# Optimization experiments

Measured on AMD Instinct MI355X. Metric: run time of the kernel, lower is better.

The kernel has to match this reference:

```python
import jax, jax.numpy as jnp
import numpy as np

NUM_HEADS = 16
NUM_HIDDENS = 1024
NEG_INF = -1e6


def setup_inputs() -> dict:
    key = jax.random.key(0)
    ks = jax.random.split(key, 8)
    B, S, D = 2, 2048, NUM_HIDDENS
    scale = 1.0 / np.sqrt(D)
    return {
        "q": jax.random.normal(ks[0], (B, S, D), jnp.float32),
        "k": jax.random.normal(ks[1], (B, S, D), jnp.float32),
        "v": jax.random.normal(ks[2], (B, S, D), jnp.float32),
        # nn.Linear weights have shape (out_features, in_features)
        "Wq": jax.random.normal(ks[3], (D, D), jnp.float32) * scale,
        "Wk": jax.random.normal(ks[4], (D, D), jnp.float32) * scale,
        "Wv": jax.random.normal(ks[5], (D, D), jnp.float32) * scale,
        "Wo": jax.random.normal(ks[6], (D, D), jnp.float32) * scale,
        "valid_len": jax.random.randint(ks[7], (B,), 1, 2048 + 1, jnp.int32),
    }


def _unpack_heads(x, nh):
    # (B, S, H) -> (B*nh, S, H//nh), matching Unpack_base_head
    B, S, H = x.shape
    return x.reshape(B, S, nh, H // nh).transpose(0, 2, 1, 3).reshape(B * nh, S, H // nh)


def _merge_heads(x, nh):
    # Faithful to Merge_base_head: (B*nh, S, dh) -> (B, nh, S, dh)
    # -> permute(0,2,3,1) -> (B, S, dh, nh) -> (B, S, dh*nh)
    Bnh, S, dh = x.shape
    B = Bnh // nh
    x = x.reshape(B, nh, S, dh).transpose(0, 2, 3, 1)
    return x.reshape(B, S, dh * nh)


def reference(q, k, v, Wq, Wk, Wv, Wo, valid_len):
    nh = NUM_HEADS
    # projections (bias=False); Linear: x @ W.T
    qh = _unpack_heads(q @ Wq.T, nh)  # (B*nh, S, dh)
    kh = _unpack_heads(k @ Wk.T, nh)
    vh = _unpack_heads(v @ Wv.T, nh)
    dh = qh.shape[-1]
    scores = jnp.einsum("bqd,bkd->bqk", qh, kh) / jnp.sqrt(jnp.float32(dh))
    # repeat_interleave valid_len by num_heads along dim 0
    vl = jnp.repeat(valid_len, nh)  # (B*nh,)
    key_pos = jnp.arange(scores.shape[-1])  # (S,)
    mask = key_pos[None, None, :] < vl[:, None, None]  # (B*nh, 1, S)
    scores = jnp.where(mask, scores, NEG_INF)
    attn = jax.nn.softmax(scores, axis=-1)  # dropout=0.0 (eval) -> identity
    out = jnp.einsum("bqk,bkd->bqd", attn, vh)  # (B*nh, S, dh)
    out = _merge_heads(out, nh) @ Wo.T  # (B, S, H)
    return out, attn
```

## Files before the change

### kernel.cpp

```cpp
#include <hip/hip_runtime.h>
#include <stdint.h>

#define SB 2048
#define DB 1024
#define NHB 16
#define DHB 64

typedef __attribute__((ext_vector_type(8))) short short8;
typedef __attribute__((ext_vector_type(4))) float f32x4;

__device__ __forceinline__ unsigned short f2bf(float f) {
  union { float f; uint32_t u; } v; v.f = f;
  uint32_t u = v.u;
  return (unsigned short)((u + 0x7FFFu + ((u >> 16) & 1u)) >> 16);
}

__device__ __forceinline__ void gld16(const void* g, void* l) {
  __builtin_amdgcn_global_load_lds(
      (const __attribute__((address_space(1))) void*)g,
      (__attribute__((address_space(3))) void*)l, 16, 0, 0);
}

__device__ __forceinline__ int xcd_swz(int bid, int nwg) {
  return (bid & 7) * (nwg >> 3) + (bid >> 3);
}

struct ConvArgs {
  const float* s[7];
  unsigned short* d[7];
  int n[7];
};

__global__ __launch_bounds__(256) void conv_kernel(ConvArgs a) {
  const int t = blockIdx.y;
  const float* __restrict__ src = a.s[t];
  unsigned short* __restrict__ dst = a.d[t];
  const int n8 = a.n[t] >> 3;
  for (int i = blockIdx.x * 256 + threadIdx.x; i < n8; i += gridDim.x * 256) {
    const f32x4* p = (const f32x4*)src + (size_t)i * 2;
    f32x4 x = p[0], y = p[1];
    short8 o;
    o[0] = (short)f2bf(x[0]); o[1] = (short)f2bf(x[1]);
    o[2] = (short)f2bf(x[2]); o[3] = (short)f2bf(x[3]);
    o[4] = (short)f2bf(y[0]); o[5] = (short)f2bf(y[1]);
    o[6] = (short)f2bf(y[2]); o[7] = (short)f2bf(y[3]);
    *(short8*)(dst + (size_t)i * 8) = o;
  }
}

struct ProjArgs {
  const unsigned short* A[3];
  const unsigned short* B[3];
  unsigned short* O[3];
};

__global__ __launch_bounds__(256) void proj_gemm(ProjArgs pa) {
  __shared__ unsigned short SH[12288];
  unsigned short* Ab = SH;
  unsigned short* Bb = SH + 8192;

  const int z = blockIdx.y;
  const unsigned short* __restrict__ A = pa.A[z];
  const unsigned short* __restrict__ Bw = pa.B[z];
  unsigned short* __restrict__ O = pa.O[z];

  const int tid = threadIdx.x;
  const int w = tid >> 6, lane = tid & 63;
  const int g = lane >> 4, li = lane & 15;
  const int wm = w >> 1, wn = w & 1;
  const int l = xcd_swz(blockIdx.x, 512);
  const int m0 = (l >> 4) * 128, n0 = (l & 15) * 64;

  const int srow = lane >> 3;
  const int sg = (lane & 7) ^ srow;

  int a_off[4][2], b_off[2][2];
  #pragma unroll
  for (int mf = 0; mf < 4; ++mf) {
    int row = wm * 64 + mf * 16 + li;
    #pragma unroll
    for (int ks = 0; ks < 2; ++ks)
      a_off[mf][ks] = row * 64 + (((ks * 4 + g) ^ (li & 7)) << 3);
  }
  #pragma unroll
  for (int nf = 0; nf < 2; ++nf) {
    int row = wn * 32 + nf * 16 + li;
    #pragma unroll
    for (int ks = 0; ks < 2; ++ks)
      b_off[nf][ks] = row * 64 + (((ks * 4 + g) ^ (li & 7)) << 3);
  }

  f32x4 acc[4][2];
  #pragma unroll
  for (int i = 0; i < 4; ++i)
    #pragma unroll
    for (int j = 0; j < 2; ++j)
      #pragma unroll
      for (int e = 0; e < 4; ++e) acc[i][j][e] = 0.f;

  for (int k0 = 0; k0 < DB; k0 += 64) {
    __syncthreads();
    #pragma unroll
    for (int i = 0; i < 4; ++i) {
      int c = w * 4 + i;
      gld16(A + (size_t)(m0 + c * 8 + srow) * DB + k0 + sg * 8, Ab + c * 512);
    }
    #pragma unroll
    for (int i = 0; i < 2; ++i) {
      int c = w * 2 + i;
      gld16(Bw + (size_t)(n0 + c * 8 + srow) * DB + k0 + sg * 8, Bb + c * 512);
    }
    __syncthreads();
    short8 af[4][2], bf[2][2];
    #pragma unroll
    for (int mf = 0; mf < 4; ++mf)
      #pragma unroll
      for (int ks = 0; ks < 2; ++ks)
        af[mf][ks] = *(const short8*)&Ab[a_off[mf][ks]];
    #pragma unroll
    for (int nf = 0; nf < 2; ++nf)
      #pragma unroll
      for (int ks = 0; ks < 2; ++ks)
        bf[nf][ks] = *(const short8*)&Bb[b_off[nf][ks]];
    #pragma unroll
    for (int ks = 0; ks < 2; ++ks)
      #pragma unroll
      for (int mf = 0; mf < 4; ++mf)
        #pragma unroll
        for (int nf = 0; nf < 2; ++nf)
          acc[mf][nf] = __builtin_amdgcn_mfma_f32_16x16x32_bf16(
              af[mf][ks], bf[nf][ks], acc[mf][nf], 0, 0, 0);
  }

  const int h = n0 >> 6;
  if (z < 2) {
    #pragma unroll
    for (int mf = 0; mf < 4; ++mf)
      #pragma unroll
      for (int nf = 0; nf < 2; ++nf)
        #pragma unroll
        for (int r = 0; r < 4; ++r) {
          int row = m0 + wm * 64 + mf * 16 + g * 4 + r;
          int col = n0 + wn * 32 + nf * 16 + li;
          int b_ = row >> 11, s_ = row & 2047, dp = col & 63;
          O[((size_t)(b_ * NHB + h) * SB + s_) * DHB + dp] = f2bf(acc[mf][nf][r]);
        }
  } else {
    __syncthreads();
    #pragma unroll
    for (int mf = 0; mf < 4; ++mf)
      #pragma unroll
      for (int nf = 0; nf < 2; ++nf)
        #pragma unroll
        for (int r = 0; r < 4; ++r)
          SH[(wm * 64 + mf * 16 + g * 4 + r) * 72 + wn * 32 + nf * 16 + li] =
              f2bf(acc[mf][nf][r]);
    __syncthreads();
    int dp = tid >> 2, ss = tid & 3;
    int b_ = m0 >> 11, s0 = (m0 & 2047) + ss * 32;
    unsigned short* dst = O + ((size_t)(b_ * NHB + h) * DHB + dp) * SB + s0;
    #pragma unroll
    for (int j2 = 0; j2 < 4; ++j2) {
      short8 o;
      #pragma unroll
      for (int j = 0; j < 8; ++j) o[j] = (short)SH[(ss * 32 + j2 * 8 + j) * 72 + dp];
      *(short8*)(dst + j2 * 8) = o;
    }
  }
}

__global__ __launch_bounds__(256) void attn_kernel(
    const unsigned short* __restrict__ Qh, const unsigned short* __restrict__ Kh,
    const unsigned short* __restrict__ Vt, const int* __restrict__ valid_len,
    float* __restrict__ attn_out, unsigned short* __restrict__ Mg)
{
  __shared__ unsigned short Klds[64][72];
  __shared__ unsigned short Vlds[64][72];
  __shared__ unsigned short QP[128][72];

  const int tid = threadIdx.x;
  const int wave = tid >> 6, lane = tid & 63;
  const int g = lane >> 4, li = lane & 15;
  const int lsw = xcd_swz(blockIdx.x, 512);
  const int q0 = (lsw & 15) * 128;
  const int bh = lsw >> 4;
  const int b_ = bh >> 4;
  const int vl = valid_len[b_];
  const int nkt = min(32, (vl + 63) >> 6);

  {
    int qr = tid >> 1, half = (tid & 1) * 32;
    const unsigned short* src = Qh + ((size_t)bh * SB + q0 + qr) * DHB + half;
    #pragma unroll
    for (int j = 0; j < 4; ++j)
      *(short8*)&QP[qr][half + j * 8] = *(const short8*)(src + j * 8);
  }
  __syncthreads();

  short8 qa[2][2];
  #pragma unroll
  for (int qf = 0; qf < 2; ++qf)
    #pragma unroll
    for (int ks = 0; ks < 2; ++ks)
      qa[qf][ks] = *(const short8*)&QP[wave * 32 + qf * 16 + li][ks * 32 + g * 8];

  float mrow[2][4], lrow[2][4];
  #pragma unroll
  for (int qf = 0; qf < 2; ++qf)
    #pragma unroll
    for (int r = 0; r < 4; ++r) { mrow[qf][r] = -1e30f; lrow[qf][r] = 0.f; }

  for (int kti = 0; kti < nkt; ++kti) {
    const int kt = kti * 64;
    __syncthreads();
    {
      int kr = tid >> 2, cs = (tid & 3) * 16;
      const unsigned short* src = Kh + ((size_t)bh * SB + kt + kr) * DHB + cs;
      *(short8*)&Klds[kr][cs]     = *(const short8*)src;
      *(short8*)&Klds[kr][cs + 8] = *(const short8*)(src + 8);
    }
    __syncthreads();
    f32x4 sc[2][4];
    #pragma unroll
    for (int qf = 0; qf < 2; ++qf)
      #pragma unroll
      for (int nf = 0; nf < 4; ++nf)
        #pragma unroll
        for (int j = 0; j < 4; ++j) sc[qf][nf][j] = 0.f;
    #pragma unroll
    for (int ks = 0; ks < 2; ++ks)
      #pragma unroll
      for (int nf = 0; nf < 4; ++nf) {
        short8 kb = *(const short8*)&Klds[nf * 16 + li][ks * 32 + g * 8];
        #pragma unroll
        for (int qf = 0; qf < 2; ++qf)
          sc[qf][nf] = __builtin_amdgcn_mfma_f32_16x16x32_bf16(qa[qf][ks], kb, sc[qf][nf], 0, 0, 0);
      }
    #pragma unroll
    for (int qf = 0; qf < 2; ++qf)
      #pragma unroll
      for (int r = 0; r < 4; ++r) {
        float sv[4], tm = -1e30f;
        #pragma unroll
        for (int nf = 0; nf < 4; ++nf) {
          int key = kt + nf * 16 + li;
          float s = sc[qf][nf][r] * 0.125f;
          s = (key < vl) ? s : -1e6f;
          sv[nf] = s;
          tm = fmaxf(tm, s);
        }
        float mo = mrow[qf][r];
        float mn = fmaxf(mo, tm);
        float la = lrow[qf][r] * __expf(mo - mn);
        #pragma unroll
        for (int nf = 0; nf < 4; ++nf) la += __expf(sv[nf] - mn);
        lrow[qf][r] = la;
        mrow[qf][r] = mn;
      }
  }

  float rl[2][4];
  #pragma unroll
  for (int qf = 0; qf < 2; ++qf)
    #pragma unroll
    for (int r = 0; r < 4; ++r) {
      float M = mrow[qf][r];
      #pragma unroll
      for (int d = 1; d < 16; d <<= 1) M = fmaxf(M, __shfl_xor(M, d));
      float L = lrow[qf][r] * __expf(mrow[qf][r] - M);
      #pragma unroll
      for (int d = 1; d < 16; d <<= 1) L += __shfl_xor(L, d);
      mrow[qf][r] = M;
      rl[qf][r] = 1.f / L;
    }

  f32x4 oacc[2][4];
  #pragma unroll
  for (int qf = 0; qf < 2; ++qf)
    #pragma unroll
    for (int nf = 0; nf < 4; ++nf)
      #pragma unroll
      for (int j = 0; j < 4; ++j) oacc[qf][nf][j] = 0.f;

  for (int kti = 0; kti < nkt; ++kti) {
    const int kt = kti * 64;
    __syncthreads();
    {
      int kr = tid >> 2, cs = (tid & 3) * 16;
      const unsigned short* src = Kh + ((size_t)bh * SB + kt + kr) * DHB + cs;
      *(short8*)&Klds[kr][cs]     = *(const short8*)src;
      *(short8*)&Klds[kr][cs + 8] = *(const short8*)(src + 8);
      const unsigned short* vs = Vt + ((size_t)bh * DHB + kr) * SB + kt + cs;
      *(short8*)&Vlds[kr][cs]     = *(const short8*)vs;
      *(short8*)&Vlds[kr][cs + 8] = *(const short8*)(vs + 8);
    }
    __syncthreads();
    f32x4 sc[2][4];
    #pragma unroll
    for (int qf = 0; qf < 2; ++qf)
      #pragma unroll
      for (int nf = 0; nf < 4; ++nf)
        #pragma unroll
        for (int j = 0; j < 4; ++j) sc[qf][nf][j] = 0.f;
    #pragma unroll
    for (int ks = 0; ks < 2; ++ks)
      #pragma unroll
      for (int nf = 0; nf < 4; ++nf) {
        short8 kb = *(const short8*)&Klds[nf * 16 + li][ks * 32 + g * 8];
        #pragma unroll
        for (int qf = 0; qf < 2; ++qf)
          sc[qf][nf] = __builtin_amdgcn_mfma_f32_16x16x32_bf16(qa[qf][ks], kb, sc[qf][nf], 0, 0, 0);
      }
    #pragma unroll
    for (int qf = 0; qf < 2; ++qf)
      #pragma unroll
      for (int nf = 0; nf < 4; ++nf)
        #pragma unroll
        for (int r = 0; r < 4; ++r) {
          int key = kt + nf * 16 + li;
          float s = sc[qf][nf][r] * 0.125f;
          s = (key < vl) ? s : -1e6f;
          float p = __expf(s - mrow[qf][r]) * rl[qf][r];
          int qrow = q0 + wave * 32 + qf * 16 + g * 4 + r;
          __builtin_nontemporal_store(
              p, attn_out + (size_t)bh * SB * SB + (size_t)qrow * SB + key);
          QP[wave * 32 + qf * 16 + g * 4 + r][nf * 16 + li] = f2bf(p);
        }
    __syncthreads();
    #pragma unroll
    for (int ks = 0; ks < 2; ++ks) {
      short8 vb[4];
      #pragma unroll
      for (int nf = 0; nf < 4; ++nf)
        vb[nf] = *(const short8*)&Vlds[nf * 16 + li][ks * 32 + g * 8];
      #pragma unroll
      for (int qf = 0; qf < 2; ++qf) {
        short8 pa = *(const short8*)&QP[wave * 32 + qf * 16 + li][ks * 32 + g * 8];
        #pragma unroll
        for (int nf = 0; nf < 4; ++nf)
          oacc[qf][nf] = __builtin_amdgcn_mfma_f32_16x16x32_bf16(pa, vb[nf], oacc[qf][nf], 0, 0, 0);
      }
    }
  }

  {
    int c0 = nkt * 64;
    int rem4 = (SB - c0) >> 2;
    if (rem4 > 0) {
      f32x4 z;
      z[0] = 0.f; z[1] = 0.f; z[2] = 0.f; z[3] = 0.f;
      for (int row = 0; row < 128; ++row) {
        float* dst = attn_out + (size_t)bh * SB * SB + (size_t)(q0 + row) * SB + c0;
        for (int c = tid; c < rem4; c += 256)
          __builtin_nontemporal_store(z, (f32x4*)dst + c);
      }
    }
  }

  const int h = bh & 15;
  #pragma unroll
  for (int qf = 0; qf < 2; ++qf)
    #pragma unroll
    for (int nf = 0; nf < 4; ++nf)
      #pragma unroll
      for (int r = 0; r < 4; ++r) {
        int qrow = q0 + wave * 32 + qf * 16 + g * 4 + r;
        int dp = nf * 16 + li;
        Mg[((size_t)b_ * SB + qrow) * DB + dp * NHB + h] = f2bf(oacc[qf][nf][r]);
      }
}

__global__ __launch_bounds__(256) void out_gemm(
    const unsigned short* __restrict__ A, const unsigned short* __restrict__ Bw,
    float* __restrict__ Out)
{
  __shared__ unsigned short SH[12288];
  unsigned short* Ab = SH;
  unsigned short* Bb = SH + 8192;

  const int tid = threadIdx.x;
  const int w = tid >> 6, lane = tid & 63;
  const int g = lane >> 4, li = lane & 15;
  const int wm = w >> 1, wn = w & 1;
  const int l = xcd_swz(blockIdx.x, 512);
  const int m0 = (l >> 4) * 128, n0 = (l & 15) * 64;

  const int srow = lane >> 3;
  const int sg = (lane & 7) ^ srow;

  int a_off[4][2], b_off[2][2];
  #pragma unroll
  for (int mf = 0; mf < 4; ++mf) {
    int row = wm * 64 + mf * 16 + li;
    #pragma unroll
    for (int ks = 0; ks < 2; ++ks)
      a_off[mf][ks] = row * 64 + (((ks * 4 + g) ^ (li & 7)) << 3);
  }
  #pragma unroll
  for (int nf = 0; nf < 2; ++nf) {
    int row = wn * 32 + nf * 16 + li;
    #pragma unroll
    for (int ks = 0; ks < 2; ++ks)
      b_off[nf][ks] = row * 64 + (((ks * 4 + g) ^ (li & 7)) << 3);
  }

  f32x4 acc[4][2];
  #pragma unroll
  for (int i = 0; i < 4; ++i)
    #pragma unroll
    for (int j = 0; j < 2; ++j)
      #pragma unroll
      for (int e = 0; e < 4; ++e) acc[i][j][e] = 0.f;

  for (int k0 = 0; k0 < DB; k0 += 64) {
    __syncthreads();
    #pragma unroll
    for (int i = 0; i < 4; ++i) {
      int c = w * 4 + i;
      gld16(A + (size_t)(m0 + c * 8 + srow) * DB + k0 + sg * 8, Ab + c * 512);
    }
    #pragma unroll
    for (int i = 0; i < 2; ++i) {
      int c = w * 2 + i;
      gld16(Bw + (size_t)(n0 + c * 8 + srow) * DB + k0 + sg * 8, Bb + c * 512);
    }
    __syncthreads();
    short8 af[4][2], bf[2][2];
    #pragma unroll
    for (int mf = 0; mf < 4; ++mf)
      #pragma unroll
      for (int ks = 0; ks < 2; ++ks)
        af[mf][ks] = *(const short8*)&Ab[a_off[mf][ks]];
    #pragma unroll
    for (int nf = 0; nf < 2; ++nf)
      #pragma unroll
      for (int ks = 0; ks < 2; ++ks)
        bf[nf][ks] = *(const short8*)&Bb[b_off[nf][ks]];
    #pragma unroll
    for (int ks = 0; ks < 2; ++ks)
      #pragma unroll
      for (int mf = 0; mf < 4; ++mf)
        #pragma unroll
        for (int nf = 0; nf < 2; ++nf)
          acc[mf][nf] = __builtin_amdgcn_mfma_f32_16x16x32_bf16(
              af[mf][ks], bf[nf][ks], acc[mf][nf], 0, 0, 0);
  }

  #pragma unroll
  for (int mf = 0; mf < 4; ++mf)
    #pragma unroll
    for (int nf = 0; nf < 2; ++nf)
      #pragma unroll
      for (int r = 0; r < 4; ++r) {
        int row = m0 + wm * 64 + mf * 16 + g * 4 + r;
        int col = n0 + wn * 32 + nf * 16 + li;
        Out[(size_t)row * DB + col] = acc[mf][nf][r];
      }
}

extern "C" void kernel_launch(void* const* d_in, const int* in_sizes, int n_in,
                              void* d_out, int out_size, void* d_ws, size_t ws_size,
                              hipStream_t stream) {
  const float* q  = (const float*)d_in[0];
  const float* k  = (const float*)d_in[1];
  const float* v  = (const float*)d_in[2];
  const float* Wq = (const float*)d_in[3];
  const float* Wk = (const float*)d_in[4];
  const float* Wv = (const float*)d_in[5];
  const float* Wo = (const float*)d_in[6];
  const int* vlen = (const int*)d_in[7];

  const size_t HS = (size_t)2 * NHB * SB * DHB;
  const size_t WS = (size_t)DB * DB;

  unsigned short* ws = (unsigned short*)d_ws;
  unsigned short* qb  = ws;
  unsigned short* kb  = qb + HS;
  unsigned short* vb  = kb + HS;
  unsigned short* Wqb = vb + HS;
  unsigned short* Wkb = Wqb + WS;
  unsigned short* Wvb = Wkb + WS;
  unsigned short* Wob = Wvb + WS;
  unsigned short* Qh  = Wob + WS;
  unsigned short* Kh  = Qh + HS;
  unsigned short* Vt  = Kh + HS;
  unsigned short* Mg  = qb;

  float* out  = (float*)d_out;
  float* attn = out + (size_t)2 * SB * DB;

  ConvArgs ca;
  ca.s[0] = q;  ca.d[0] = qb;  ca.n[0] = (int)HS;
  ca.s[1] = k;  ca.d[1] = kb;  ca.n[1] = (int)HS;
  ca.s[2] = v;  ca.d[2] = vb;  ca.n[2] = (int)HS;
  ca.s[3] = Wq; ca.d[3] = Wqb; ca.n[3] = (int)WS;
  ca.s[4] = Wk; ca.d[4] = Wkb; ca.n[4] = (int)WS;
  ca.s[5] = Wv; ca.d[5] = Wvb; ca.n[5] = (int)WS;
  ca.s[6] = Wo; ca.d[6] = Wob; ca.n[6] = (int)WS;

  ProjArgs pa;
  pa.A[0] = qb;  pa.A[1] = kb;  pa.A[2] = vb;
  pa.B[0] = Wqb; pa.B[1] = Wkb; pa.B[2] = Wvb;
  pa.O[0] = Qh;  pa.O[1] = Kh;  pa.O[2] = Vt;

  dim3 blk(256);
  conv_kernel<<<dim3(1024, 7), blk, 0, stream>>>(ca);
  proj_gemm<<<dim3(512, 3), blk, 0, stream>>>(pa);
  attn_kernel<<<dim3(512), blk, 0, stream>>>(Qh, Kh, Vt, vlen, attn, Mg);
  out_gemm<<<dim3(512), blk, 0, stream>>>(Mg, Wob, out);
}
```

Baseline: 248.9 us.

## Unify GEMMs into 128x128 tiles and pipeline attention K/V loads

```diff
diff --git a/kernel.cpp b/kernel.cpp
--- a/kernel.cpp
+++ b/kernel.cpp
@@ -7,6 +7,7 @@
 #define DHB 64
 
 typedef __attribute__((ext_vector_type(8))) short short8;
+typedef __attribute__((ext_vector_type(4))) short short4v;
 typedef __attribute__((ext_vector_type(4))) float f32x4;
 
 __device__ __forceinline__ unsigned short f2bf(float f) {
@@ -48,53 +49,38 @@
   }
 }
 
-struct ProjArgs {
+struct GemmArgs {
   const unsigned short* A[3];
   const unsigned short* B[3];
-  unsigned short* O[3];
+  void* O[3];
+  int mode[3];
 };
 
-__global__ __launch_bounds__(256) void proj_gemm(ProjArgs pa) {
-  __shared__ unsigned short SH[12288];
+__global__ __launch_bounds__(256) void gemm128(GemmArgs ga) {
+  __shared__ unsigned short SH[17408];
   unsigned short* Ab = SH;
   unsigned short* Bb = SH + 8192;
 
   const int z = blockIdx.y;
-  const unsigned short* __restrict__ A = pa.A[z];
-  const unsigned short* __restrict__ Bw = pa.B[z];
-  unsigned short* __restrict__ O = pa.O[z];
+  const unsigned short* __restrict__ A = ga.A[z];
+  const unsigned short* __restrict__ Bw = ga.B[z];
+  const int mode = ga.mode[z];
 
   const int tid = threadIdx.x;
   const int w = tid >> 6, lane = tid & 63;
   const int g = lane >> 4, li = lane & 15;
   const int wm = w >> 1, wn = w & 1;
-  const int l = xcd_swz(blockIdx.x, 512);
-  const int m0 = (l >> 4) * 128, n0 = (l & 15) * 64;
+  const int l = xcd_swz(blockIdx.x, 256);
+  const int m0 = (l >> 3) * 128, n0 = (l & 7) * 128;
 
   const int srow = lane >> 3;
   const int sg = (lane & 7) ^ srow;
 
-  int a_off[4][2], b_off[2][2];
-  #pragma unroll
-  for (int mf = 0; mf < 4; ++mf) {
-    int row = wm * 64 + mf * 16 + li;
-    #pragma unroll
-    for (int ks = 0; ks < 2; ++ks)
-      a_off[mf][ks] = row * 64 + (((ks * 4 + g) ^ (li & 7)) << 3);
-  }
-  #pragma unroll
-  for (int nf = 0; nf < 2; ++nf) {
-    int row = wn * 32 + nf * 16 + li;
-    #pragma unroll
-    for (int ks = 0; ks < 2; ++ks)
-      b_off[nf][ks] = row * 64 + (((ks * 4 + g) ^ (li & 7)) << 3);
-  }
-
-  f32x4 acc[4][2];
+  f32x4 acc[4][4];
   #pragma unroll
   for (int i = 0; i < 4; ++i)
     #pragma unroll
-    for (int j = 0; j < 2; ++j)
+    for (int j = 0; j < 4; ++j)
       #pragma unroll
       for (int e = 0; e < 4; ++e) acc[i][j][e] = 0.f;
 
@@ -104,68 +90,80 @@
     for (int i = 0; i < 4; ++i) {
       int c = w * 4 + i;
       gld16(A + (size_t)(m0 + c * 8 + srow) * DB + k0 + sg * 8, Ab + c * 512);
-    }
-    #pragma unroll
-    for (int i = 0; i < 2; ++i) {
-      int c = w * 2 + i;
       gld16(Bw + (size_t)(n0 + c * 8 + srow) * DB + k0 + sg * 8, Bb + c * 512);
     }
     __syncthreads();
-    short8 af[4][2], bf[2][2];
+    short8 af[4][2], bf[4][2];
     #pragma unroll
     for (int mf = 0; mf < 4; ++mf)
       #pragma unroll
       for (int ks = 0; ks < 2; ++ks)
-        af[mf][ks] = *(const short8*)&Ab[a_off[mf][ks]];
-    #pragma unroll
-    for (int nf = 0; nf < 2; ++nf)
+        af[mf][ks] = *(const short8*)&Ab[(wm * 64 + mf * 16 + li) * 64 +
+                                         (((ks * 4 + g) ^ (li & 7)) << 3)];
+    #pragma unroll
+    for (int nf = 0; nf < 4; ++nf)
       #pragma unroll
       for (int ks = 0; ks < 2; ++ks)
-        bf[nf][ks] = *(const short8*)&Bb[b_off[nf][ks]];
+        bf[nf][ks] = *(const short8*)&Bb[(wn * 64 + nf * 16 + li) * 64 +
+                                         (((ks * 4 + g) ^ (li & 7)) << 3)];
     #pragma unroll
     for (int ks = 0; ks < 2; ++ks)
       #pragma unroll
       for (int mf = 0; mf < 4; ++mf)
         #pragma unroll
-        for (int nf = 0; nf < 2; ++nf)
+        for (int nf = 0; nf < 4; ++nf)
           acc[mf][nf] = __builtin_amdgcn_mfma_f32_16x16x32_bf16(
               af[mf][ks], bf[nf][ks], acc[mf][nf], 0, 0, 0);
   }
 
-  const int h = n0 >> 6;
-  if (z < 2) {
+  if (mode == 0) {
+    unsigned short* O = (unsigned short*)ga.O[z];
     #pragma unroll
     for (int mf = 0; mf < 4; ++mf)
       #pragma unroll
-      for (int nf = 0; nf < 2; ++nf)
+      for (int nf = 0; nf < 4; ++nf)
         #pragma unroll
         for (int r = 0; r < 4; ++r) {
           int row = m0 + wm * 64 + mf * 16 + g * 4 + r;
-          int col = n0 + wn * 32 + nf * 16 + li;
-          int b_ = row >> 11, s_ = row & 2047, dp = col & 63;
+          int col = n0 + wn * 64 + nf * 16 + li;
+          int b_ = row >> 11, s_ = row & 2047;
+          int h = col >> 6, dp = col & 63;
           O[((size_t)(b_ * NHB + h) * SB + s_) * DHB + dp] = f2bf(acc[mf][nf][r]);
         }
+  } else if (mode == 1) {
+    unsigned short* O = (unsigned short*)ga.O[z];
+    __syncthreads();
+    #pragma unroll
+    for (int mf = 0; mf < 4; ++mf)
+      #pragma unroll
+      for (int nf = 0; nf < 4; ++nf) {
+        short4v pk;
+        #pragma unroll
+        for (int r = 0; r < 4; ++r) pk[r] = (short)f2bf(acc[mf][nf][r]);
+        *(short4v*)&SH[(size_t)(wn * 64 + nf * 16 + li) * 136 +
+                       wm * 64 + mf * 16 + g * 4] = pk;
+      }
+    __syncthreads();
+    int c = tid >> 1, rh = tid & 1;
+    int col = n0 + c;
+    int h = col >> 6, dp = col & 63;
+    int b_ = m0 >> 11, s0 = (m0 & 2047) + rh * 64;
+    unsigned short* dst = O + ((size_t)(b_ * NHB + h) * DHB + dp) * SB + s0;
+    #pragma unroll
+    for (int j = 0; j < 8; ++j)
+      *(short8*)(dst + j * 8) = *(const short8*)&SH[c * 136 + rh * 64 + j * 8];
   } else {
-    __syncthreads();
+    float* O = (float*)ga.O[z];
     #pragma unroll
     for (int mf = 0; mf < 4; ++mf)
       #pragma unroll
-      for (int nf = 0; nf < 2; ++nf)
-        #pragma unroll
-        for (int r = 0; r < 4; ++r)
-          SH[(wm * 64 + mf * 16 + g * 4 + r) * 72 + wn * 32 + nf * 16 + li] =
-              f2bf(acc[mf][nf][r]);
-    __syncthreads();
-    int dp = tid >> 2, ss = tid & 3;
-    int b_ = m0 >> 11, s0 = (m0 & 2047) + ss * 32;
-    unsigned short* dst = O + ((size_t)(b_ * NHB + h) * DHB + dp) * SB + s0;
-    #pragma unroll
-    for (int j2 = 0; j2 < 4; ++j2) {
-      short8 o;
-      #pragma unroll
-      for (int j = 0; j < 8; ++j) o[j] = (short)SH[(ss * 32 + j2 * 8 + j) * 72 + dp];
-      *(short8*)(dst + j2 * 8) = o;
-    }
+      for (int nf = 0; nf < 4; ++nf)
+        #pragma unroll
+        for (int r = 0; r < 4; ++r) {
+          int row = m0 + wm * 64 + mf * 16 + g * 4 + r;
+          int col = n0 + wn * 64 + nf * 16 + li;
+          O[(size_t)row * DB + col] = acc[mf][nf][r];
+        }
   }
 }
 
@@ -174,8 +172,8 @@
     const unsigned short* __restrict__ Vt, const int* __restrict__ valid_len,
     float* __restrict__ attn_out, unsigned short* __restrict__ Mg)
 {
-  __shared__ unsigned short Klds[64][72];
-  __shared__ unsigned short Vlds[64][72];
+  __shared__ unsigned short Kb[2][4096];
+  __shared__ unsigned short Vb[2][4096];
   __shared__ unsigned short QP[128][72];
 
   const int tid = threadIdx.x;
@@ -188,6 +186,9 @@
   const int vl = valid_len[b_];
   const int nkt = min(32, (vl + 63) >> 6);
 
+  const int srow = lane >> 3;
+  const int sg = (lane & 7) ^ srow;
+
   {
     int qr = tid >> 1, half = (tid & 1) * 32;
     const unsigned short* src = Qh + ((size_t)bh * SB + q0 + qr) * DHB + half;
@@ -204,75 +205,84 @@
     for (int ks = 0; ks < 2; ++ks)
       qa[qf][ks] = *(const short8*)&QP[wave * 32 + qf * 16 + li][ks * 32 + g * 8];
 
-  float mrow[2][4], lrow[2][4];
+  float mQ[2] = {-1e30f, -1e30f}, lQ[2] = {0.f, 0.f};
+
+  {
+    #pragma unroll
+    for (int i = 0; i < 2; ++i) {
+      int c = wave * 2 + i;
+      gld16(Kh + ((size_t)bh * SB + 0 + c * 8 + srow) * DHB + sg * 8,
+            &Kb[0][c * 512]);
+    }
+    int cur = 0;
+    for (int kti = 0; kti < nkt; ++kti) {
+      const int kt = kti * 64;
+      __syncthreads();
+      if (kti + 1 < nkt) {
+        #pragma unroll
+        for (int i = 0; i < 2; ++i) {
+          int c = wave * 2 + i;
+          gld16(Kh + ((size_t)bh * SB + kt + 64 + c * 8 + srow) * DHB + sg * 8,
+                &Kb[cur ^ 1][c * 512]);
+        }
+      }
+      f32x4 sc[2][4];
+      #pragma unroll
+      for (int qf = 0; qf < 2; ++qf)
+        #pragma unroll
+        for (int nf = 0; nf < 4; ++nf)
+          #pragma unroll
+          for (int j = 0; j < 4; ++j) sc[qf][nf][j] = 0.f;
+      #pragma unroll
+      for (int ks = 0; ks < 2; ++ks)
+        #pragma unroll
+        for (int nf = 0; nf < 4; ++nf) {
+          short8 kbf = *(const short8*)&Kb[cur][(nf * 16 + li) * 64 +
+                                               (((ks * 4 + g) ^ (li & 7)) << 3)];
+          #pragma unroll
+          for (int qf = 0; qf < 2; ++qf)
+            sc[qf][nf] = __builtin_amdgcn_mfma_f32_16x16x32_bf16(
+                kbf, qa[qf][ks], sc[qf][nf], 0, 0, 0);
+        }
+      #pragma unroll
+      for (int qf = 0; qf < 2; ++qf) {
+        float tm = -1e30f;
+        #pragma unroll
+        for (int nf = 0; nf < 4; ++nf)
+          #pragma unroll
+          for (int r = 0; r < 4; ++r) {
+            int key = kt + nf * 16 + g * 4 + r;
+            float s = sc[qf][nf][r] * 0.125f;
+            s = (key < vl) ? s : -1e6f;
+            sc[qf][nf][r] = s;
+            tm = fmaxf(tm, s);
+          }
+        float mo = mQ[qf], mn = fmaxf(mo, tm);
+        float la = lQ[qf] * __expf(mo - mn);
+        #pragma unroll
+        for (int nf = 0; nf < 4; ++nf)
+          #pragma unroll
+          for (int r = 0; r < 4; ++r) la += __expf(sc[qf][nf][r] - mn);
+        mQ[qf] = mn;
+        lQ[qf] = la;
+      }
+      cur ^= 1;
+    }
+  }
+  __syncthreads();
+
+  float rlQ[2];
   #pragma unroll
-  for (int qf = 0; qf < 2; ++qf)
-    #pragma unroll
-    for (int r = 0; r < 4; ++r) { mrow[qf][r] = -1e30f; lrow[qf][r] = 0.f; }
-
-  for (int kti = 0; kti < nkt; ++kti) {
-    const int kt = kti * 64;
-    __syncthreads();
-    {
-      int kr = tid >> 2, cs = (tid & 3) * 16;
-      const unsigned short* src = Kh + ((size_t)bh * SB + kt + kr) * DHB + cs;
-      *(short8*)&Klds[kr][cs]     = *(const short8*)src;
-      *(short8*)&Klds[kr][cs + 8] = *(const short8*)(src + 8);
-    }
-    __syncthreads();
-    f32x4 sc[2][4];
-    #pragma unroll
-    for (int qf = 0; qf < 2; ++qf)
-      #pragma unroll
-      for (int nf = 0; nf < 4; ++nf)
-        #pragma unroll
-        for (int j = 0; j < 4; ++j) sc[qf][nf][j] = 0.f;
-    #pragma unroll
-    for (int ks = 0; ks < 2; ++ks)
-      #pragma unroll
-      for (int nf = 0; nf < 4; ++nf) {
-        short8 kb = *(const short8*)&Klds[nf * 16 + li][ks * 32 + g * 8];
-        #pragma unroll
-        for (int qf = 0; qf < 2; ++qf)
-          sc[qf][nf] = __builtin_amdgcn_mfma_f32_16x16x32_bf16(qa[qf][ks], kb, sc[qf][nf], 0, 0, 0);
-      }
-    #pragma unroll
-    for (int qf = 0; qf < 2; ++qf)
-      #pragma unroll
-      for (int r = 0; r < 4; ++r) {
-        float sv[4], tm = -1e30f;
-        #pragma unroll
-        for (int nf = 0; nf < 4; ++nf) {
-          int key = kt + nf * 16 + li;
-          float s = sc[qf][nf][r] * 0.125f;
-          s = (key < vl) ? s : -1e6f;
-          sv[nf] = s;
-          tm = fmaxf(tm, s);
-        }
-        float mo = mrow[qf][r];
-        float mn = fmaxf(mo, tm);
-        float la = lrow[qf][r] * __expf(mo - mn);
-        #pragma unroll
-        for (int nf = 0; nf < 4; ++nf) la += __expf(sv[nf] - mn);
-        lrow[qf][r] = la;
-        mrow[qf][r] = mn;
-      }
-  }
-
-  float rl[2][4];
-  #pragma unroll
-  for (int qf = 0; qf < 2; ++qf)
-    #pragma unroll
-    for (int r = 0; r < 4; ++r) {
-      float M = mrow[qf][r];
-      #pragma unroll
-      for (int d = 1; d < 16; d <<= 1) M = fmaxf(M, __shfl_xor(M, d));
-      float L = lrow[qf][r] * __expf(mrow[qf][r] - M);
-      #pragma unroll
-      for (int d = 1; d < 16; d <<= 1) L += __shfl_xor(L, d);
-      mrow[qf][r] = M;
-      rl[qf][r] = 1.f / L;
-    }
+  for (int qf = 0; qf < 2; ++qf) {
+    float M = mQ[qf];
+    M = fmaxf(M, __shfl_xor(M, 16));
+    M = fmaxf(M, __shfl_xor(M, 32));
+    float L = lQ[qf] * __expf(mQ[qf] - M);
+    L += __shfl_xor(L, 16);
+    L += __shfl_xor(L, 32);
+    mQ[qf] = M;
+    rlQ[qf] = 1.f / L;
+  }
 
   f32x4 oacc[2][4];
   #pragma unroll
@@ -282,64 +292,86 @@
       #pragma unroll
       for (int j = 0; j < 4; ++j) oacc[qf][nf][j] = 0.f;
 
-  for (int kti = 0; kti < nkt; ++kti) {
-    const int kt = kti * 64;
-    __syncthreads();
-    {
-      int kr = tid >> 2, cs = (tid & 3) * 16;
-      const unsigned short* src = Kh + ((size_t)bh * SB + kt + kr) * DHB + cs;
-      *(short8*)&Klds[kr][cs]     = *(const short8*)src;
-      *(short8*)&Klds[kr][cs + 8] = *(const short8*)(src + 8);
-      const unsigned short* vs = Vt + ((size_t)bh * DHB + kr) * SB + kt + cs;
-      *(short8*)&Vlds[kr][cs]     = *(const short8*)vs;
-      *(short8*)&Vlds[kr][cs + 8] = *(const short8*)(vs + 8);
-    }
-    __syncthreads();
-    f32x4 sc[2][4];
-    #pragma unroll
-    for (int qf = 0; qf < 2; ++qf)
-      #pragma unroll
-      for (int nf = 0; nf < 4; ++nf)
-        #pragma unroll
-        for (int j = 0; j < 4; ++j) sc[qf][nf][j] = 0.f;
-    #pragma unroll
-    for (int ks = 0; ks < 2; ++ks)
-      #pragma unroll
-      for (int nf = 0; nf < 4; ++nf) {
-        short8 kb = *(const short8*)&Klds[nf * 16 + li][ks * 32 + g * 8];
-        #pragma unroll
-        for (int qf = 0; qf < 2; ++qf)
-          sc[qf][nf] = __builtin_amdgcn_mfma_f32_16x16x32_bf16(qa[qf][ks], kb, sc[qf][nf], 0, 0, 0);
-      }
-    #pragma unroll
-    for (int qf = 0; qf < 2; ++qf)
-      #pragma unroll
-      for (int nf = 0; nf < 4; ++nf)
-        #pragma unroll
-        for (int r = 0; r < 4; ++r) {
-          int key = kt + nf * 16 + li;
-          float s = sc[qf][nf][r] * 0.125f;
-          s = (key < vl) ? s : -1e6f;
-          float p = __expf(s - mrow[qf][r]) * rl[qf][r];
-          int qrow = q0 + wave * 32 + qf * 16 + g * 4 + r;
+  {
+    #pragma unroll
+    for (int i = 0; i < 2; ++i) {
+      int c = wave * 2 + i;
+      gld16(Kh + ((size_t)bh * SB + c * 8 + srow) * DHB + sg * 8, &Kb[0][c * 512]);
+      gld16(Vt + ((size_t)bh * DHB + c * 8 + srow) * SB + 0 + sg * 8, &Vb[0][c * 512]);
+    }
+    int cur = 0;
+    for (int kti = 0; kti < nkt; ++kti) {
+      const int kt = kti * 64;
+      __syncthreads();
+      if (kti + 1 < nkt) {
+        #pragma unroll
+        for (int i = 0; i < 2; ++i) {
+          int c = wave * 2 + i;
+          gld16(Kh + ((size_t)bh * SB + kt + 64 + c * 8 + srow) * DHB + sg * 8,
+                &Kb[cur ^ 1][c * 512]);
+          gld16(Vt + ((size_t)bh * DHB + c * 8 + srow) * SB + kt + 64 + sg * 8,
+                &Vb[cur ^ 1][c * 512]);
+        }
+      }
+      f32x4 sc[2][4];
+      #pragma unroll
+      for (int qf = 0; qf < 2; ++qf)
+        #pragma unroll
+        for (int nf = 0; nf < 4; ++nf)
+          #pragma unroll
+          for (int j = 0; j < 4; ++j) sc[qf][nf][j] = 0.f;
+      #pragma unroll
+      for (int ks = 0; ks < 2; ++ks)
+        #pragma unroll
+        for (int nf = 0; nf < 4; ++nf) {
+          short8 kbf = *(const short8*)&Kb[cur][(nf * 16 + li) * 64 +
+                                               (((ks * 4 + g) ^ (li & 7)) << 3)];
+          #pragma unroll
+          for (int qf = 0; qf < 2; ++qf)
+            sc[qf][nf] = __builtin_amdgcn_mfma_f32_16x16x32_bf16(
+                kbf, qa[qf][ks], sc[qf][nf], 0, 0, 0);
+        }
+      #pragma unroll
+      for (int qf = 0; qf < 2; ++qf) {
+        int qrow = q0 + wave * 32 + qf * 16 + li;
+        #pragma unroll
+        for (int nf = 0; nf < 4; ++nf) {
+          short4v pk;
+          #pragma unroll
+          for (int r = 0; r < 4; ++r) {
+            int key = kt + nf * 16 + g * 4 + r;
+            float s = sc[qf][nf][r] * 0.125f;
+            s = (key < vl) ? s : -1e6f;
+            float p = __expf(s - mQ[qf]) * rlQ[qf];
+            sc[qf][nf][r] = p;
+            pk[r] = (short)f2bf(p);
+          }
           __builtin_nontemporal_store(
-              p, attn_out + (size_t)bh * SB * SB + (size_t)qrow * SB + key);
-          QP[wave * 32 + qf * 16 + g * 4 + r][nf * 16 + li] = f2bf(p);
-        }
-    __syncthreads();
-    #pragma unroll
-    for (int ks = 0; ks < 2; ++ks) {
-      short8 vb[4];
-      #pragma unroll
-      for (int nf = 0; nf < 4; ++nf)
-        vb[nf] = *(const short8*)&Vlds[nf * 16 + li][ks * 32 + g * 8];
-      #pragma unroll
-      for (int qf = 0; qf < 2; ++qf) {
-        short8 pa = *(const short8*)&QP[wave * 32 + qf * 16 + li][ks * 32 + g * 8];
-        #pragma unroll
-        for (int nf = 0; nf < 4; ++nf)
-          oacc[qf][nf] = __builtin_amdgcn_mfma_f32_16x16x32_bf16(pa, vb[nf], oacc[qf][nf], 0, 0, 0);
-      }
+              sc[qf][nf],
+              (f32x4*)(attn_out + (size_t)bh * SB * SB + (size_t)qrow * SB +
+                       kt + nf * 16 + g * 4));
+          *(short4v*)&QP[wave * 32 + qf * 16 + li][nf * 16 + g * 4] = pk;
+        }
+      }
+      asm volatile("s_waitcnt lgkmcnt(0)" ::: "memory");
+      __builtin_amdgcn_sched_barrier(0);
+      #pragma unroll
+      for (int ks = 0; ks < 2; ++ks) {
+        short8 vbf[4];
+        #pragma unroll
+        for (int nf = 0; nf < 4; ++nf)
+          vbf[nf] = *(const short8*)&Vb[cur][(nf * 16 + li) * 64 +
+                                             (((ks * 4 + g) ^ (li & 7)) << 3)];
+        #pragma unroll
+        for (int qf = 0; qf < 2; ++qf) {
+          short8 pa = *(const short8*)&QP[wave * 32 + qf * 16 + li][ks * 32 + g * 8];
+          #pragma unroll
+          for (int nf = 0; nf < 4; ++nf)
+            oacc[qf][nf] = __builtin_amdgcn_mfma_f32_16x16x32_bf16(
+                pa, vbf[nf], oacc[qf][nf], 0, 0, 0);
+        }
+      }
+      cur ^= 1;
     }
   }
 
@@ -367,94 +399,6 @@
         int qrow = q0 + wave * 32 + qf * 16 + g * 4 + r;
         int dp = nf * 16 + li;
         Mg[((size_t)b_ * SB + qrow) * DB + dp * NHB + h] = f2bf(oacc[qf][nf][r]);
-      }
-}
-
-__global__ __launch_bounds__(256) void out_gemm(
-    const unsigned short* __restrict__ A, const unsigned short* __restrict__ Bw,
-    float* __restrict__ Out)
-{
-  __shared__ unsigned short SH[12288];
-  unsigned short* Ab = SH;
-  unsigned short* Bb = SH + 8192;
-
-  const int tid = threadIdx.x;
-  const int w = tid >> 6, lane = tid & 63;
-  const int g = lane >> 4, li = lane & 15;
-  const int wm = w >> 1, wn = w & 1;
-  const int l = xcd_swz(blockIdx.x, 512);
-  const int m0 = (l >> 4) * 128, n0 = (l & 15) * 64;
-
-  const int srow = lane >> 3;
-  const int sg = (lane & 7) ^ srow;
-
-  int a_off[4][2], b_off[2][2];
-  #pragma unroll
-  for (int mf = 0; mf < 4; ++mf) {
-    int row = wm * 64 + mf * 16 + li;
-    #pragma unroll
-    for (int ks = 0; ks < 2; ++ks)
-      a_off[mf][ks] = row * 64 + (((ks * 4 + g) ^ (li & 7)) << 3);
-  }
-  #pragma unroll
-  for (int nf = 0; nf < 2; ++nf) {
-    int row = wn * 32 + nf * 16 + li;
-    #pragma unroll
-    for (int ks = 0; ks < 2; ++ks)
-      b_off[nf][ks] = row * 64 + (((ks * 4 + g) ^ (li & 7)) << 3);
-  }
-
-  f32x4 acc[4][2];
-  #pragma unroll
-  for (int i = 0; i < 4; ++i)
-    #pragma unroll
-    for (int j = 0; j < 2; ++j)
-      #pragma unroll
-      for (int e = 0; e < 4; ++e) acc[i][j][e] = 0.f;
-
-  for (int k0 = 0; k0 < DB; k0 += 64) {
-    __syncthreads();
-    #pragma unroll
-    for (int i = 0; i < 4; ++i) {
-      int c = w * 4 + i;
-      gld16(A + (size_t)(m0 + c * 8 + srow) * DB + k0 + sg * 8, Ab + c * 512);
-    }
-    #pragma unroll
-    for (int i = 0; i < 2; ++i) {
-      int c = w * 2 + i;
-      gld16(Bw + (size_t)(n0 + c * 8 + srow) * DB + k0 + sg * 8, Bb + c * 512);
-    }
-    __syncthreads();
-    short8 af[4][2], bf[2][2];
-    #pragma unroll
-    for (int mf = 0; mf < 4; ++mf)
-      #pragma unroll
-      for (int ks = 0; ks < 2; ++ks)
-        af[mf][ks] = *(const short8*)&Ab[a_off[mf][ks]];
-    #pragma unroll
-    for (int nf = 0; nf < 2; ++nf)
-      #pragma unroll
-      for (int ks = 0; ks < 2; ++ks)
-        bf[nf][ks] = *(const short8*)&Bb[b_off[nf][ks]];
-    #pragma unroll
-    for (int ks = 0; ks < 2; ++ks)
-      #pragma unroll
-      for (int mf = 0; mf < 4; ++mf)
-        #pragma unroll
-        for (int nf = 0; nf < 2; ++nf)
-          acc[mf][nf] = __builtin_amdgcn_mfma_f32_16x16x32_bf16(
-              af[mf][ks], bf[nf][ks], acc[mf][nf], 0, 0, 0);
-  }
-
-  #pragma unroll
-  for (int mf = 0; mf < 4; ++mf)
-    #pragma unroll
-    for (int nf = 0; nf < 2; ++nf)
-      #pragma unroll
-      for (int r = 0; r < 4; ++r) {
-        int row = m0 + wm * 64 + mf * 16 + g * 4 + r;
-        int col = n0 + wn * 32 + nf * 16 + li;
-        Out[(size_t)row * DB + col] = acc[mf][nf][r];
       }
 }
 
@@ -498,14 +442,20 @@
   ca.s[5] = Wv; ca.d[5] = Wvb; ca.n[5] = (int)WS;
   ca.s[6] = Wo; ca.d[6] = Wob; ca.n[6] = (int)WS;
 
-  ProjArgs pa;
+  GemmArgs pa;
   pa.A[0] = qb;  pa.A[1] = kb;  pa.A[2] = vb;
   pa.B[0] = Wqb; pa.B[1] = Wkb; pa.B[2] = Wvb;
   pa.O[0] = Qh;  pa.O[1] = Kh;  pa.O[2] = Vt;
+  pa.mode[0] = 0; pa.mode[1] = 0; pa.mode[2] = 1;
+
+  GemmArgs oa;
+  oa.A[0] = Mg; oa.B[0] = Wob; oa.O[0] = out; oa.mode[0] = 2;
+  oa.A[1] = Mg; oa.B[1] = Wob; oa.O[1] = out; oa.mode[1] = 2;
+  oa.A[2] = Mg; oa.B[2] = Wob; oa.O[2] = out; oa.mode[2] = 2;
 
   dim3 blk(256);
   conv_kernel<<<dim3(1024, 7), blk, 0, stream>>>(ca);
-  proj_gemm<<<dim3(512, 3), blk, 0, stream>>>(pa);
+  gemm128<<<dim3(256, 3), blk, 0, stream>>>(pa);
   attn_kernel<<<dim3(512), blk, 0, stream>>>(Qh, Kh, Vt, vlen, attn, Mg);
-  out_gemm<<<dim3(512), blk, 0, stream>>>(Mg, Wob, out);
-}
+  gemm128<<<dim3(256, 1), blk, 0, stream>>>(oa);
+}
```

After: 256.8 us. 1.03x slower.
